# Performance work log

Measured on AMD Instinct MI355X. Metric: run time of the kernel, lower is better.

## Reference

```python
import jax, jax.numpy as jnp
import numpy as np

B, TE, TD, D = 32, 2048, 64, 1024

def setup_inputs() -> dict:
    key = jax.random.key(0)
    k1, k2, k3, k4, k5 = jax.random.split(key, 5)
    return {
        "encoder_outputs": jax.random.normal(k1, (B, TE, D), dtype=jnp.float32),
        "decoder_outputs": jax.random.normal(k2, (B, TD, D), dtype=jnp.float32),
        "W_a": jax.random.normal(k3, (D, D), dtype=jnp.float32) * (1.0 / np.sqrt(D)),
        "U_a": jax.random.normal(k4, (D, D), dtype=jnp.float32) * (1.0 / np.sqrt(D)),
        "V_a": jax.random.normal(k5, (D, 1), dtype=jnp.float32) * (1.0 / np.sqrt(D)),
    }

def reference(encoder_outputs, decoder_outputs, W_a, U_a, V_a):
    # Bahdanau additive attention over encoder positions, query = last decoder step.
    dec_last = decoder_outputs[:, -1, :]                      # [B, D]
    enc_W = jnp.einsum('bte,ef->btf', encoder_outputs, W_a)   # [B, Te, D]
    dec_U = jnp.einsum('bd,df->bf', dec_last, U_a)            # [B, D] (broadcast over Te instead of tile)
    tanh_out = jnp.tanh(enc_W + dec_U[:, None, :])            # [B, Te, D]
    scores = jnp.einsum('btf,fo->bt', tanh_out, V_a[:, 0:1])  # [B, Te] (squeeze of [B,Te,1])
    weights = jax.nn.softmax(scores, axis=1)                  # [B, Te]
    context = jnp.einsum('bte,bt->be', encoder_outputs, weights)  # [B, D]
    return context, weights[..., None]
```

## Files before the change

kernel.cpp:

```cpp
#include <hip/hip_runtime.h>
#include <stdint.h>

typedef __attribute__((ext_vector_type(8))) __bf16 bf16x8;
typedef __attribute__((ext_vector_type(4))) float  f32x4;

__device__ __forceinline__ uint16_t f2b(float f) {
  uint32_t u = __float_as_uint(f);
  u += 0x7fffu + ((u >> 16) & 1u);
  return (uint16_t)(u >> 16);
}
__device__ __forceinline__ float b2f_lo(uint32_t p) { return __uint_as_float(p << 16); }
__device__ __forceinline__ float b2f_hi(uint32_t p) { return __uint_as_float(p & 0xffff0000u); }

__device__ __forceinline__ float tanh_fast(float x) {
  float e = __expf(2.0f * x);
  return 1.0f - 2.0f / (e + 1.0f);
}

__device__ __forceinline__ void bar() { asm volatile("s_barrier" ::: "memory"); }
__device__ __forceinline__ void wait_vm0() { asm volatile("s_waitcnt vmcnt(0)" ::: "memory"); }

__device__ __forceinline__ void gload16(const void* g, void* l) {
  __builtin_amdgcn_global_load_lds(
      (__attribute__((address_space(1))) uint32_t*)g,
      (__attribute__((address_space(3))) uint32_t*)l, 16, 0, 0);
}

__global__ __launch_bounds__(256) void convert_enc(const float4* __restrict__ in,
                                                   uint4* __restrict__ out) {
  int i = blockIdx.x * 256 + threadIdx.x;
  float4 a = in[2 * i], b = in[2 * i + 1];
  uint4 o;
  o.x = (uint32_t)f2b(a.x) | ((uint32_t)f2b(a.y) << 16);
  o.y = (uint32_t)f2b(a.z) | ((uint32_t)f2b(a.w) << 16);
  o.z = (uint32_t)f2b(b.x) | ((uint32_t)f2b(b.y) << 16);
  o.w = (uint32_t)f2b(b.z) | ((uint32_t)f2b(b.w) << 16);
  out[i] = o;
}

__global__ __launch_bounds__(256) void convert_WT(const float* __restrict__ W,
                                                  uint16_t* __restrict__ WT) {
  __shared__ float tile[64][65];
  int k0 = (blockIdx.x & 15) * 64;
  int n0 = (blockIdx.x >> 4) * 64;
  #pragma unroll
  for (int it = 0; it < 16; ++it) {
    int idx = it * 256 + threadIdx.x;
    int kr = idx >> 6, nc = idx & 63;
    tile[kr][nc] = W[(size_t)(k0 + kr) * 1024 + n0 + nc];
  }
  __syncthreads();
  #pragma unroll
  for (int it = 0; it < 16; ++it) {
    int idx = it * 256 + threadIdx.x;
    int nr = idx >> 6, kc = idx & 63;
    WT[(size_t)(n0 + nr) * 1024 + k0 + kc] = f2b(tile[kc][nr]);
  }
}

__global__ __launch_bounds__(256) void compute_u(const float* __restrict__ dec,
                                                 const float4* __restrict__ U4,
                                                 float* __restrict__ u) {
  int b = blockIdx.x >> 3, dseg = blockIdx.x & 7;
  __shared__ float sdec[128];
  if (threadIdx.x < 128)
    sdec[threadIdx.x] = dec[(size_t)b * 64 * 1024 + 63 * 1024 + dseg * 128 + threadIdx.x];
  __syncthreads();
  float4 a = {0.f, 0.f, 0.f, 0.f};
  const float4* Ub = U4 + (size_t)dseg * 128 * 256 + threadIdx.x;
  #pragma unroll 4
  for (int d = 0; d < 128; ++d) {
    float4 w = Ub[(size_t)d * 256];
    float s = sdec[d];
    a.x = fmaf(s, w.x, a.x);
    a.y = fmaf(s, w.y, a.y);
    a.z = fmaf(s, w.z, a.z);
    a.w = fmaf(s, w.w, a.w);
  }
  float* up = u + b * 1024 + threadIdx.x * 4;
  atomicAdd(up + 0, a.x);
  atomicAdd(up + 1, a.y);
  atomicAdd(up + 2, a.z);
  atomicAdd(up + 3, a.w);
}

__global__ __launch_bounds__(512, 2) void gemm_score(const uint16_t* __restrict__ A,
                                                     const uint16_t* __restrict__ BT,
                                                     const float* __restrict__ u,
                                                     const float* __restrict__ v,
                                                     float* __restrict__ spart) {
  __shared__ uint4 lds4[2][4][1024];
  __shared__ float sred[4][256];

  const int bx = blockIdx.x;
  const int wg = (bx & 7) * 128 + (bx >> 3);
  const int mtile = wg >> 2;
  const int ntile = wg & 3;

  const int tid = threadIdx.x;
  const int lane = tid & 63;
  const int wid = tid >> 6;
  const int wr = wid >> 2;
  const int wc = wid & 3;
  const int nib = lane & 15;
  const int q4 = lane >> 4;

  const int rowA = mtile * 256;
  const char* baseA = (const char*)A + (size_t)rowA * 2048;
  const char* baseB = (const char*)BT + (size_t)ntile * 256 * 2048;
  const size_t rowoff = (size_t)(tid >> 3) * 2048 +
                        (size_t)(((tid & 7) ^ ((tid >> 3) & 7)) << 4);

#define STAGE2(nbuf, h, srcbase)                                      \
  do {                                                                \
    const char* _s = (srcbase);                                       \
    gload16(_s + rowoff,             &lds4[nbuf][h][wid * 64]);       \
    gload16(_s + rowoff + 64 * 2048, &lds4[nbuf][h][512 + wid * 64]); \
  } while (0)

  f32x4 acc[8][4];
  #pragma unroll
  for (int i = 0; i < 8; ++i)
    #pragma unroll
    for (int j = 0; j < 4; ++j) acc[i][j] = (f32x4){0.f, 0.f, 0.f, 0.f};

  STAGE2(0, 0, baseA);
  STAGE2(0, 1, baseA + 128 * 2048);
  STAGE2(0, 2, baseB);
  STAGE2(0, 3, baseB + 128 * 2048);
  wait_vm0();
  bar();

  bf16x8 bfr[4];
  const int bhalf = 2 + (wc >> 1);
  const int ncol0 = (wc & 1) * 64;

  #pragma unroll 2
  for (int kt = 0; kt < 16; ++kt) {
    const int cb = kt & 1, nb = cb ^ 1;
    const char* nA = baseA + (size_t)(kt + 1) * 128;
    const char* nB = baseB + (size_t)(kt + 1) * 128;
    #pragma unroll
    for (int q = 0; q < 4; ++q) {
      const int qi = q & 1, kk = q >> 1;
      const int kx = (kk * 4 + q4) ^ (nib & 7);
      bf16x8 af[4];
      #pragma unroll
      for (int i = 0; i < 4; ++i)
        af[i] = *(const bf16x8*)&lds4[cb][wr][(qi * 64 + i * 16 + nib) * 8 + kx];
      if (qi == 0) {
        #pragma unroll
        for (int j = 0; j < 4; ++j)
          bfr[j] = *(const bf16x8*)&lds4[cb][bhalf][(ncol0 + j * 16 + nib) * 8 + kx];
      }
      if (kt < 15) {
        if (q == 0) {
          STAGE2(nb, 0, nA);
          STAGE2(nb, 1, nA + 128 * 2048);
        } else if (q == 1) {
          STAGE2(nb, 2, nB);
          STAGE2(nb, 3, nB + 128 * 2048);
        }
      }
      bar();
      __builtin_amdgcn_s_setprio(1);
      #pragma unroll
      for (int i = 0; i < 4; ++i)
        #pragma unroll
        for (int j = 0; j < 4; ++j)
          acc[qi * 4 + i][j] = __builtin_amdgcn_mfma_f32_16x16x32_bf16(
              af[i], bfr[j], acc[qi * 4 + i][j], 0, 0, 0);
      __builtin_amdgcn_s_setprio(0);
      if (q == 3) wait_vm0();
      bar();
    }
  }
#undef STAGE2

  const int b = mtile >> 3;
  float vv[4], uu[4];
  #pragma unroll
  for (int j = 0; j < 4; ++j) {
    int col = ntile * 256 + wc * 64 + j * 16 + nib;
    vv[j] = v[col];
    uu[j] = u[b * 1024 + col];
  }
  #pragma unroll
  for (int qi = 0; qi < 2; ++qi)
    #pragma unroll
    for (int i = 0; i < 4; ++i)
      #pragma unroll
      for (int reg = 0; reg < 4; ++reg) {
        float s = 0.f;
        #pragma unroll
        for (int j = 0; j < 4; ++j) s += vv[j] * tanh_fast(acc[qi * 4 + i][j][reg] + uu[j]);
        s += __shfl_xor(s, 1);
        s += __shfl_xor(s, 2);
        s += __shfl_xor(s, 4);
        s += __shfl_xor(s, 8);
        if (nib == 0) sred[wc][wr * 128 + qi * 64 + i * 16 + q4 * 4 + reg] = s;
      }
  __syncthreads();
  if (tid < 256) {
    float s = sred[0][tid] + sred[1][tid] + sred[2][tid] + sred[3][tid];
    spart[(size_t)ntile * 65536 + rowA + tid] = s;
  }
}

__global__ __launch_bounds__(256) void softmax_k(const float* __restrict__ spart,
                                                 float* __restrict__ wout) {
  int b = blockIdx.x, tid = threadIdx.x;
  __shared__ float red[4];
  float sv[8];
  float mx = -1e30f;
  #pragma unroll
  for (int i = 0; i < 8; ++i) {
    int idx = b * 2048 + i * 256 + tid;
    float s = 0.f;
    #pragma unroll
    for (int j = 0; j < 4; ++j) s += spart[j * 65536 + idx];
    sv[i] = s;
    mx = fmaxf(mx, s);
  }
  #pragma unroll
  for (int off = 1; off < 64; off <<= 1) mx = fmaxf(mx, __shfl_xor(mx, off));
  if ((tid & 63) == 0) red[tid >> 6] = mx;
  __syncthreads();
  mx = fmaxf(fmaxf(red[0], red[1]), fmaxf(red[2], red[3]));
  __syncthreads();
  float sum = 0.f;
  #pragma unroll
  for (int i = 0; i < 8; ++i) {
    sv[i] = __expf(sv[i] - mx);
    sum += sv[i];
  }
  #pragma unroll
  for (int off = 1; off < 64; off <<= 1) sum += __shfl_xor(sum, off);
  if ((tid & 63) == 0) red[tid >> 6] = sum;
  __syncthreads();
  float inv = 1.0f / (red[0] + red[1] + red[2] + red[3]);
  #pragma unroll
  for (int i = 0; i < 8; ++i) wout[b * 2048 + i * 256 + tid] = sv[i] * inv;
}

__global__ __launch_bounds__(256) void context_k(const uint16_t* __restrict__ encA,
                                                 const float* __restrict__ w,
                                                 float* __restrict__ ctx) {
  int b = blockIdx.x >> 5, ch = blockIdx.x & 31;
  int t0 = ch * 64;
  __shared__ float lw[64];
  if (threadIdx.x < 64) lw[threadIdx.x] = w[b * 2048 + t0 + threadIdx.x];
  __syncthreads();
  int e0 = threadIdx.x * 4;
  float a0 = 0.f, a1 = 0.f, a2 = 0.f, a3 = 0.f;
  const uint16_t* base = encA + (size_t)b * 2048 * 1024 + (size_t)t0 * 1024 + e0;
  #pragma unroll 4
  for (int t = 0; t < 64; ++t) {
    uint2 p = *(const uint2*)(base + (size_t)t * 1024);
    float wt = lw[t];
    a0 = fmaf(wt, b2f_lo(p.x), a0);
    a1 = fmaf(wt, b2f_hi(p.x), a1);
    a2 = fmaf(wt, b2f_lo(p.y), a2);
    a3 = fmaf(wt, b2f_hi(p.y), a3);
  }
  atomicAdd(&ctx[b * 1024 + e0 + 0], a0);
  atomicAdd(&ctx[b * 1024 + e0 + 1], a1);
  atomicAdd(&ctx[b * 1024 + e0 + 2], a2);
  atomicAdd(&ctx[b * 1024 + e0 + 3], a3);
}

extern "C" void kernel_launch(void* const* d_in, const int* in_sizes, int n_in,
                              void* d_out, int out_size, void* d_ws, size_t ws_size,
                              hipStream_t stream) {
  const float* enc = (const float*)d_in[0];
  const float* dec = (const float*)d_in[1];
  const float* Wa  = (const float*)d_in[2];
  const float* Ua  = (const float*)d_in[3];
  const float* Va  = (const float*)d_in[4];

  float* out = (float*)d_out;
  float* ctx = out;
  float* wts = out + 32 * 1024;

  char* ws = (char*)d_ws;
  uint16_t* encA  = (uint16_t*)ws;
  uint16_t* WT    = (uint16_t*)(ws + 134217728);
  float*    ub    = (float*)  (ws + 136314880);
  float*    spart = (float*)  (ws + 136445952);

  hipMemsetAsync(ctx, 0, 32 * 1024 * sizeof(float), stream);
  hipMemsetAsync(ub, 0, 32 * 1024 * sizeof(float), stream);

  convert_enc<<<32768, 256, 0, stream>>>((const float4*)enc, (uint4*)encA);
  convert_WT<<<256, 256, 0, stream>>>(Wa, WT);
  compute_u<<<256, 256, 0, stream>>>(dec, (const float4*)Ua, ub);
  gemm_score<<<1024, 512, 0, stream>>>(encA, WT, ub, Va, spart);
  softmax_k<<<32, 256, 0, stream>>>(spart, wts);
  context_k<<<1024, 256, 0, stream>>>(encA, wts, ctx);
}
```

Before: 623.2 us.

## Use 4-stage LDS pipeline with 32-wide K tiles in score GEMM; widen context loads

Measured after the change: 630.5 us. No clear change (+1.2%).

```diff
diff --git a/kernel.cpp b/kernel.cpp
--- a/kernel.cpp
+++ b/kernel.cpp
@@ -18,7 +18,6 @@
 }
 
 __device__ __forceinline__ void bar() { asm volatile("s_barrier" ::: "memory"); }
-__device__ __forceinline__ void wait_vm0() { asm volatile("s_waitcnt vmcnt(0)" ::: "memory"); }
 
 __device__ __forceinline__ void gload16(const void* g, void* l) {
   __builtin_amdgcn_global_load_lds(
@@ -89,7 +88,7 @@
                                                      const float* __restrict__ u,
                                                      const float* __restrict__ v,
                                                      float* __restrict__ spart) {
-  __shared__ uint4 lds4[2][4][1024];
+  __shared__ uint4 lds4[4][2][1024];
   __shared__ float sred[4][256];
 
   const int bx = blockIdx.x;
@@ -104,18 +103,19 @@
   const int wc = wid & 3;
   const int nib = lane & 15;
   const int q4 = lane >> 4;
+  const int fx = q4 ^ ((nib >> 1) & 3);
 
   const int rowA = mtile * 256;
   const char* baseA = (const char*)A + (size_t)rowA * 2048;
   const char* baseB = (const char*)BT + (size_t)ntile * 256 * 2048;
-  const size_t rowoff = (size_t)(tid >> 3) * 2048 +
-                        (size_t)(((tid & 7) ^ ((tid >> 3) & 7)) << 4);
-
-#define STAGE2(nbuf, h, srcbase)                                      \
-  do {                                                                \
-    const char* _s = (srcbase);                                       \
-    gload16(_s + rowoff,             &lds4[nbuf][h][wid * 64]);       \
-    gload16(_s + rowoff + 64 * 2048, &lds4[nbuf][h][512 + wid * 64]); \
+  const size_t srcoff = (size_t)(tid >> 2) * 2048 +
+                        ((size_t)((tid & 3) ^ ((tid >> 3) & 3)) << 4);
+
+#define STAGE_OP(buf, op, srcbase, kt)                                        \
+  do {                                                                        \
+    const char* _s = (const char*)(srcbase) + (size_t)(kt) * 64;              \
+    gload16(_s + srcoff,              &lds4[(buf)][(op)][wid * 64]);          \
+    gload16(_s + srcoff + 128 * 2048, &lds4[(buf)][(op)][512 + wid * 64]);    \
   } while (0)
 
   f32x4 acc[8][4];
@@ -124,58 +124,52 @@
     #pragma unroll
     for (int j = 0; j < 4; ++j) acc[i][j] = (f32x4){0.f, 0.f, 0.f, 0.f};
 
-  STAGE2(0, 0, baseA);
-  STAGE2(0, 1, baseA + 128 * 2048);
-  STAGE2(0, 2, baseB);
-  STAGE2(0, 3, baseB + 128 * 2048);
-  wait_vm0();
+  STAGE_OP(0, 0, baseA, 0); STAGE_OP(0, 1, baseB, 0);
+  STAGE_OP(1, 0, baseA, 1); STAGE_OP(1, 1, baseB, 1);
+  STAGE_OP(2, 0, baseA, 2); STAGE_OP(2, 1, baseB, 2);
+  asm volatile("s_waitcnt vmcnt(8)" ::: "memory");
   bar();
 
   bf16x8 bfr[4];
-  const int bhalf = 2 + (wc >> 1);
-  const int ncol0 = (wc & 1) * 64;
-
-  #pragma unroll 2
-  for (int kt = 0; kt < 16; ++kt) {
-    const int cb = kt & 1, nb = cb ^ 1;
-    const char* nA = baseA + (size_t)(kt + 1) * 128;
-    const char* nB = baseB + (size_t)(kt + 1) * 128;
-    #pragma unroll
-    for (int q = 0; q < 4; ++q) {
-      const int qi = q & 1, kk = q >> 1;
-      const int kx = (kk * 4 + q4) ^ (nib & 7);
-      bf16x8 af[4];
-      #pragma unroll
-      for (int i = 0; i < 4; ++i)
-        af[i] = *(const bf16x8*)&lds4[cb][wr][(qi * 64 + i * 16 + nib) * 8 + kx];
-      if (qi == 0) {
-        #pragma unroll
-        for (int j = 0; j < 4; ++j)
-          bfr[j] = *(const bf16x8*)&lds4[cb][bhalf][(ncol0 + j * 16 + nib) * 8 + kx];
-      }
-      if (kt < 15) {
-        if (q == 0) {
-          STAGE2(nb, 0, nA);
-          STAGE2(nb, 1, nA + 128 * 2048);
-        } else if (q == 1) {
-          STAGE2(nb, 2, nB);
-          STAGE2(nb, 3, nB + 128 * 2048);
-        }
-      }
-      bar();
-      __builtin_amdgcn_s_setprio(1);
-      #pragma unroll
-      for (int i = 0; i < 4; ++i)
-        #pragma unroll
-        for (int j = 0; j < 4; ++j)
-          acc[qi * 4 + i][j] = __builtin_amdgcn_mfma_f32_16x16x32_bf16(
-              af[i], bfr[j], acc[qi * 4 + i][j], 0, 0, 0);
-      __builtin_amdgcn_s_setprio(0);
-      if (q == 3) wait_vm0();
-      bar();
-    }
-  }
-#undef STAGE2
+
+#define PHASE(cb_, qi_, ...)                                                  \
+  do {                                                                        \
+    bf16x8 af[4];                                                             \
+    _Pragma("unroll")                                                         \
+    for (int i = 0; i < 4; ++i)                                               \
+      af[i] = *(const bf16x8*)&lds4[cb_][0]                                   \
+              [(wr * 128 + (qi_) * 64 + i * 16 + nib) * 4 + fx];              \
+    if ((qi_) == 0) {                                                         \
+      _Pragma("unroll")                                                       \
+      for (int j = 0; j < 4; ++j)                                             \
+        bfr[j] = *(const bf16x8*)&lds4[cb_][1]                                \
+                 [(wc * 64 + j * 16 + nib) * 4 + fx];                         \
+    }                                                                         \
+    __VA_ARGS__;                                                              \
+    bar();                                                                    \
+    __builtin_amdgcn_s_setprio(1);                                            \
+    _Pragma("unroll")                                                         \
+    for (int i = 0; i < 4; ++i)                                               \
+      _Pragma("unroll")                                                       \
+      for (int j = 0; j < 4; ++j)                                             \
+        acc[(qi_) * 4 + i][j] = __builtin_amdgcn_mfma_f32_16x16x32_bf16(      \
+            af[i], bfr[j], acc[(qi_) * 4 + i][j], 0, 0, 0);                   \
+    __builtin_amdgcn_s_setprio(0);                                            \
+  } while (0)
+
+  for (int t = 0; t < 32; ++t) {
+    const int cb = t & 3, sb = (t + 3) & 3;
+    const bool st = (t < 29);
+    PHASE(cb, 0, if (st) STAGE_OP(sb, 0, baseA, t + 3));
+    bar();
+    PHASE(cb, 1, if (st) STAGE_OP(sb, 1, baseB, t + 3));
+    if (t < 29)       asm volatile("s_waitcnt vmcnt(8)" ::: "memory");
+    else if (t == 29) asm volatile("s_waitcnt vmcnt(4)" ::: "memory");
+    else if (t == 30) asm volatile("s_waitcnt vmcnt(0)" ::: "memory");
+    bar();
+  }
+#undef PHASE
+#undef STAGE_OP
 
   const int b = mtile >> 3;
   float vv[4], uu[4];
@@ -246,27 +240,33 @@
 __global__ __launch_bounds__(256) void context_k(const uint16_t* __restrict__ encA,
                                                  const float* __restrict__ w,
                                                  float* __restrict__ ctx) {
-  int b = blockIdx.x >> 5, ch = blockIdx.x & 31;
-  int t0 = ch * 64;
-  __shared__ float lw[64];
-  if (threadIdx.x < 64) lw[threadIdx.x] = w[b * 2048 + t0 + threadIdx.x];
-  __syncthreads();
-  int e0 = threadIdx.x * 4;
-  float a0 = 0.f, a1 = 0.f, a2 = 0.f, a3 = 0.f;
-  const uint16_t* base = encA + (size_t)b * 2048 * 1024 + (size_t)t0 * 1024 + e0;
-  #pragma unroll 4
+  int b = blockIdx.x >> 4, ch = blockIdx.x & 15;
+  int t0 = ch * 128;
+  __shared__ float lw[128];
+  if (threadIdx.x < 128) lw[threadIdx.x] = w[b * 2048 + t0 + threadIdx.x];
+  __syncthreads();
+  int th = threadIdx.x >> 7;
+  int i  = threadIdx.x & 127;
+  int e0 = i * 8;
+  float a[8] = {0.f, 0.f, 0.f, 0.f, 0.f, 0.f, 0.f, 0.f};
+  const uint16_t* base = encA + (size_t)b * 2048 * 1024 + (size_t)(t0 + th * 64) * 1024 + e0;
+  const float* lwp = lw + th * 64;
+  #pragma unroll 2
   for (int t = 0; t < 64; ++t) {
-    uint2 p = *(const uint2*)(base + (size_t)t * 1024);
-    float wt = lw[t];
-    a0 = fmaf(wt, b2f_lo(p.x), a0);
-    a1 = fmaf(wt, b2f_hi(p.x), a1);
-    a2 = fmaf(wt, b2f_lo(p.y), a2);
-    a3 = fmaf(wt, b2f_hi(p.y), a3);
-  }
-  atomicAdd(&ctx[b * 1024 + e0 + 0], a0);
-  atomicAdd(&ctx[b * 1024 + e0 + 1], a1);
-  atomicAdd(&ctx[b * 1024 + e0 + 2], a2);
-  atomicAdd(&ctx[b * 1024 + e0 + 3], a3);
+    uint4 p = *(const uint4*)(base + (size_t)t * 1024);
+    float wt = lwp[t];
+    a[0] = fmaf(wt, b2f_lo(p.x), a[0]);
+    a[1] = fmaf(wt, b2f_hi(p.x), a[1]);
+    a[2] = fmaf(wt, b2f_lo(p.y), a[2]);
+    a[3] = fmaf(wt, b2f_hi(p.y), a[3]);
+    a[4] = fmaf(wt, b2f_lo(p.z), a[4]);
+    a[5] = fmaf(wt, b2f_hi(p.z), a[5]);
+    a[6] = fmaf(wt, b2f_lo(p.w), a[6]);
+    a[7] = fmaf(wt, b2f_hi(p.w), a[7]);
+  }
+  float* cp = &ctx[b * 1024 + e0];
+  #pragma unroll
+  for (int k = 0; k < 8; ++k) atomicAdd(cp + k, a[k]);
 }
 
 extern "C" void kernel_launch(void* const* d_in, const int* in_sizes, int n_in,
@@ -296,5 +296,5 @@
   compute_u<<<256, 256, 0, stream>>>(dec, (const float4*)Ua, ub);
   gemm_score<<<1024, 512, 0, stream>>>(encA, WT, ub, Va, spart);
   softmax_k<<<32, 256, 0, stream>>>(spart, wts);
-  context_k<<<1024, 256, 0, stream>>>(encA, wts, ctx);
-}
+  context_k<<<512, 256, 0, stream>>>(encA, wts, ctx);
+}
```
